# Kernel tuning notes

Measured on AMD Instinct MI355X. Metric: run time of the kernel, lower is better.

Reference implementation:

```python
import jax, jax.numpy as jnp
import numpy as np

B, Q, K = 8, 1024, 1024
DQ, DK, DV, H = 64, 64, 64, 64
NEG = -1000000.0


def setup_inputs() -> dict:
    key = jax.random.key(0)
    ks = jax.random.split(key, 7)
    return {
        "queries": jax.random.normal(ks[0], (B, Q, DQ), dtype=jnp.float32),
        "keys": jax.random.normal(ks[1], (B, K, DK), dtype=jnp.float32),
        "values": jax.random.normal(ks[2], (B, K, DV), dtype=jnp.float32),
        "valid_lens": jax.random.randint(ks[3], (B,), 1, K + 1, dtype=jnp.int64).astype(jnp.int32),
        # learned params (LazyLinear, no bias)
        "W_q": jax.random.normal(ks[4], (DQ, H), dtype=jnp.float32) / np.sqrt(DQ),
        "W_k": jax.random.normal(ks[5], (DK, H), dtype=jnp.float32) / np.sqrt(DK),
        "w_v": jax.random.normal(ks[6], (H,), dtype=jnp.float32) / np.sqrt(H),
    }


def reference(queries, keys, values, valid_lens, W_q, W_k, w_v):
    q = jnp.einsum("bqd,dh->bqh", queries, W_q)            # [B,Q,H]
    k = jnp.einsum("bkd,dh->bkh", keys, W_k)               # [B,K,H]
    # broadcast-add + tanh materializes [B,Q,K,H] (faithful to original)
    features = jnp.tanh(q[:, :, None, :] + k[:, None, :, :])
    scores = jnp.einsum("bqkh,h->bqk", features, w_v)      # [B,Q,K]
    # masked softmax: valid_lens is 1-D -> broadcast over query rows
    mask = jnp.arange(scores.shape[-1])[None, None, :] < valid_lens[:, None, None]
    scores = jnp.where(mask, scores, NEG)
    attn = jax.nn.softmax(scores, axis=-1)                 # [B,Q,K]
    return jnp.einsum("bqk,bkv->bqv", attn, values)        # [B,Q,DV]
```

## Files before the change

### kernel.cpp

```cpp
#include <hip/hip_runtime.h>

#define BDIM 8
#define QDIM 1024
#define KDIM 1024
#define HDIM 64
#define KTPC 2
#define MAXCH 8

constexpr float kLog2e = 1.4426950408889634f;
constexpr float kC2 = 2.0f * kLog2e;

__global__ __launch_bounds__(256) void proj_both(
    const float* __restrict__ queries, const float* __restrict__ keys,
    const float* __restrict__ Wq, const float* __restrict__ Wk,
    float* __restrict__ eq, float* __restrict__ ek) {
  const int bid = blockIdx.x;
  const bool isK = bid >= 128;
  const float* X = isK ? keys : queries;
  const float* W = isK ? Wk : Wq;
  float* Y = isK ? ek : eq;
  const long long base = (long long)(bid & 127) * 64 * 64;

  __shared__ __align__(16) float xs[64][68];
  __shared__ __align__(16) float ws[64][64];
  const int t = threadIdx.x;
  {
    const int r = t >> 4, sl = t & 15;
#pragma unroll
    for (int i = 0; i < 4; ++i) {
      *(float4*)&xs[r + i * 16][sl * 4] =
          *(const float4*)&X[base + (long long)(r + i * 16) * 64 + sl * 4];
      *(float4*)&ws[r + i * 16][sl * 4] =
          *(const float4*)&W[(r + i * 16) * 64 + sl * 4];
    }
  }
  __syncthreads();

  const int r = t >> 2;
  const int c0 = (t & 3) * 16;
  float acc[16];
#pragma unroll
  for (int j = 0; j < 16; ++j) acc[j] = 0.0f;

#pragma unroll 8
  for (int d = 0; d < 64; ++d) {
    const float xv = xs[r][d];
#pragma unroll
    for (int j4 = 0; j4 < 4; ++j4) {
      float4 w4 = *(float4*)&ws[d][c0 + j4 * 4];
      acc[j4 * 4 + 0] = fmaf(xv, w4.x, acc[j4 * 4 + 0]);
      acc[j4 * 4 + 1] = fmaf(xv, w4.y, acc[j4 * 4 + 1]);
      acc[j4 * 4 + 2] = fmaf(xv, w4.z, acc[j4 * 4 + 2]);
      acc[j4 * 4 + 3] = fmaf(xv, w4.w, acc[j4 * 4 + 3]);
    }
  }
#pragma unroll
  for (int j4 = 0; j4 < 4; ++j4) {
    float4 o = make_float4(
        fminf(__builtin_amdgcn_exp2f(acc[j4 * 4 + 0] * kC2), 32768.0f),
        fminf(__builtin_amdgcn_exp2f(acc[j4 * 4 + 1] * kC2), 32768.0f),
        fminf(__builtin_amdgcn_exp2f(acc[j4 * 4 + 2] * kC2), 32768.0f),
        fminf(__builtin_amdgcn_exp2f(acc[j4 * 4 + 3] * kC2), 32768.0f));
    *(float4*)&Y[base + (long long)r * 64 + c0 + j4 * 4] = o;
  }
}

__global__ __launch_bounds__(256, 3) void fused_kernel(
    const float* __restrict__ eqp, const float* __restrict__ ekp,
    const float* __restrict__ vglob, const float* __restrict__ wv,
    const int* __restrict__ vlens, float* __restrict__ part_o,
    float2* __restrict__ part_ml) {
  int pre[9];
  pre[0] = 0;
#pragma unroll
  for (int bb = 0; bb < 8; ++bb) {
    int nt = (vlens[bb] + 63) >> 6;
    nt = nt < 16 ? nt : 16;
    const int nch = (nt + KTPC - 1) / KTPC;
    pre[bb + 1] = pre[bb] + (nch << 6);
  }
  const int g = blockIdx.x;
  if (g >= pre[8]) return;
  int b = 0;
#pragma unroll
  for (int i = 0; i < 7; ++i) b += (g >= pre[i + 1]);
  const int local = g - pre[b];
  const int qt = local & 63;
  const int ch = local >> 6;
  const int q0 = qt * 16;
  const int vlen = vlens[b];
  int nt = (vlen + 63) >> 6;
  nt = nt < 16 ? nt : 16;
  const int kt0 = ch * KTPC;
  const int ktend = (kt0 + KTPC < nt) ? kt0 + KTPC : nt;

  __shared__ __align__(16) float qs[16][64];
  __shared__ __align__(16) float ks[64][64];
  __shared__ __align__(16) float vs[64][64];
  __shared__ __align__(16) float ps[16][68];
  const int t = threadIdx.x;
  const int tq = t >> 4;
  const int kg = t & 15;
  const int kbs = kg << 2;
  const int key0 = ((kbs + 0) ^ kg) & 15;
  const int key1 = ((kbs + 1) ^ kg) & 15;
  const int key2 = ((kbs + 2) ^ kg) & 15;
  const int key3 = ((kbs + 3) ^ kg) & 15;

  float sumw = 0.0f;
#pragma unroll
  for (int h = 0; h < 64; ++h) sumw += wv[h];

  {
    const int r = t >> 4, sl = t & 15;
    *(float4*)&qs[r][sl * 4] =
        *(const float4*)&eqp[(long long)(b * QDIM + q0 + r) * 64 + sl * 4];
  }

  float4 o4 = make_float4(0.0f, 0.0f, 0.0f, 0.0f);
  float m = -3.0e38f, l = 0.0f;

  for (int kt = kt0; kt < ktend; ++kt) {
    __syncthreads();
#pragma unroll
    for (int i = 0; i < 4; ++i) {
      const int f = i * 256 + t;
      const int k = f >> 4, sl = f & 15;
      const int key = (k ^ (k >> 2)) & 15;
      const long long grow = (long long)(b * KDIM + kt * 64 + k) * 64 + sl * 4;
      *(float4*)&ks[k][(sl ^ key) * 4] = *(const float4*)&ekp[grow];
      *(float4*)&vs[k][sl * 4] = *(const float4*)&vglob[grow];
    }
    __syncthreads();

    float acc0 = 0.0f, acc1 = 0.0f, acc2 = 0.0f, acc3 = 0.0f;
    float4 qA, kA0, kA1, kA2, kA3;
    float4 qB, kB0, kB1, kB2, kB3;

#define LOAD_STAGE(QF, K0, K1, K2, K3, H)                  \
  QF = *(const float4*)&qs[tq][(H) * 4];                   \
  K0 = *(const float4*)&ks[kbs + 0][((H) ^ key0) * 4];     \
  K1 = *(const float4*)&ks[kbs + 1][((H) ^ key1) * 4];     \
  K2 = *(const float4*)&ks[kbs + 2][((H) ^ key2) * 4];     \
  K3 = *(const float4*)&ks[kbs + 3][((H) ^ key3) * 4];

#define QUAD(ACC, QF, KF, W0, W1, W2, W3)                  \
  {                                                        \
    const float u0 = fmaf(QF.x, KF.x, 1.0f);               \
    const float u1 = fmaf(QF.y, KF.y, 1.0f);               \
    const float u2 = fmaf(QF.z, KF.z, 1.0f);               \
    const float u3 = fmaf(QF.w, KF.w, 1.0f);               \
    const float d01 = u0 * u1;                             \
    const float d23 = u2 * u3;                             \
    const float n01 = fmaf(W1, u0, W0 * u1);               \
    const float n23 = fmaf(W3, u2, W2 * u3);               \
    const float num = fmaf(n23, d01, n01 * d23);           \
    ACC = fmaf(num, __builtin_amdgcn_rcpf(d01 * d23), ACC);\
  }

#define COMP_STAGE(QF, K0, K1, K2, K3, H)                  \
  {                                                        \
    const float w0 = wv[(H) * 4 + 0];                      \
    const float w1 = wv[(H) * 4 + 1];                      \
    const float w2 = wv[(H) * 4 + 2];                      \
    const float w3 = wv[(H) * 4 + 3];                      \
    QUAD(acc0, QF, K0, w0, w1, w2, w3)                     \
    QUAD(acc1, QF, K1, w0, w1, w2, w3)                     \
    QUAD(acc2, QF, K2, w0, w1, w2, w3)                     \
    QUAD(acc3, QF, K3, w0, w1, w2, w3)                     \
  }

    LOAD_STAGE(qA, kA0, kA1, kA2, kA3, 0)
#pragma unroll
    for (int h = 0; h < 16; h += 2) {
      LOAD_STAGE(qB, kB0, kB1, kB2, kB3, h + 1)
      COMP_STAGE(qA, kA0, kA1, kA2, kA3, h)
      if (h + 2 < 16) LOAD_STAGE(qA, kA0, kA1, kA2, kA3, h + 2)
      COMP_STAGE(qB, kB0, kB1, kB2, kB3, h + 1)
    }
#undef LOAD_STAGE
#undef COMP_STAGE
#undef QUAD

    const int kgl = kt * 64 + kbs;
    float s0 = fmaf(-2.0f, acc0, sumw);
    float s1 = fmaf(-2.0f, acc1, sumw);
    float s2 = fmaf(-2.0f, acc2, sumw);
    float s3 = fmaf(-2.0f, acc3, sumw);
    s0 = (kgl + 0 < vlen) ? s0 : -3.0e38f;
    s1 = (kgl + 1 < vlen) ? s1 : -3.0e38f;
    s2 = (kgl + 2 < vlen) ? s2 : -3.0e38f;
    s3 = (kgl + 3 < vlen) ? s3 : -3.0e38f;
    float tm = fmaxf(fmaxf(s0, s1), fmaxf(s2, s3));
#pragma unroll
    for (int s = 1; s < 16; s <<= 1) tm = fmaxf(tm, __shfl_xor(tm, s, 64));
    const float mn = fmaxf(m, tm);
    const float scale = __builtin_amdgcn_exp2f((m - mn) * kLog2e);
    const float p0 = __builtin_amdgcn_exp2f((s0 - mn) * kLog2e);
    const float p1 = __builtin_amdgcn_exp2f((s1 - mn) * kLog2e);
    const float p2 = __builtin_amdgcn_exp2f((s2 - mn) * kLog2e);
    const float p3 = __builtin_amdgcn_exp2f((s3 - mn) * kLog2e);
    float tsum = (p0 + p1) + (p2 + p3);
#pragma unroll
    for (int s = 1; s < 16; s <<= 1) tsum += __shfl_xor(tsum, s, 64);
    l = fmaf(l, scale, tsum);
    m = mn;
    o4.x *= scale; o4.y *= scale; o4.z *= scale; o4.w *= scale;
    *(float4*)&ps[tq][kbs] = make_float4(p0, p1, p2, p3);
    __syncthreads();

#pragma unroll 4
    for (int k4 = 0; k4 < 16; ++k4) {
      const float4 p4 = *(const float4*)&ps[tq][k4 * 4];
      const float pw[4] = {p4.x, p4.y, p4.z, p4.w};
#pragma unroll
      for (int e = 0; e < 4; ++e) {
        const float4 vv = *(const float4*)&vs[k4 * 4 + e][kbs];
        o4.x = fmaf(pw[e], vv.x, o4.x);
        o4.y = fmaf(pw[e], vv.y, o4.y);
        o4.z = fmaf(pw[e], vv.z, o4.z);
        o4.w = fmaf(pw[e], vv.w, o4.w);
      }
    }
  }

  *(float4*)&part_o[((long long)g * 16 + tq) * 64 + kbs] = o4;
  if (kg == 0) part_ml[g * 16 + tq] = make_float2(m, l);
}

__global__ __launch_bounds__(256) void combine_kernel(
    const float* __restrict__ part_o, const float2* __restrict__ part_ml,
    const int* __restrict__ vlens, float* __restrict__ out) {
  int pre[8], nchv[8];
  int run = 0;
#pragma unroll
  for (int bb = 0; bb < 8; ++bb) {
    int nt = (vlens[bb] + 63) >> 6;
    nt = nt < 16 ? nt : 16;
    nchv[bb] = (nt + KTPC - 1) / KTPC;
    pre[bb] = run;
    run += nchv[bb] << 6;
  }
  const int t = threadIdx.x;
  const int row = blockIdx.x * 4 + (t >> 6);
  const int lane = t & 63;
  const int b = row >> 10;
  const int q = row & (QDIM - 1);
  const int qt = q >> 4;
  const int tq = q & 15;
  const int nch = nchv[b];
  const int slot0 = pre[b] + qt;

  float M = -3.0e38f;
  float mv[MAXCH], lv[MAXCH];
#pragma unroll
  for (int c = 0; c < MAXCH; ++c) {
    if (c < nch) {
      const float2 ml = part_ml[(slot0 + (c << 6)) * 16 + tq];
      mv[c] = ml.x;
      lv[c] = ml.y;
      M = fmaxf(M, ml.x);
    }
  }
  float L = 0.0f, acc = 0.0f;
#pragma unroll
  for (int c = 0; c < MAXCH; ++c) {
    if (c < nch) {
      const float w = __builtin_amdgcn_exp2f((mv[c] - M) * kLog2e);
      L = fmaf(lv[c], w, L);
      const float ov =
          part_o[((long long)(slot0 + (c << 6)) * 16 + tq) * 64 + lane];
      acc = fmaf(ov, w, acc);
    }
  }
  out[(long long)row * 64 + lane] = acc * __builtin_amdgcn_rcpf(L);
}

extern "C" void kernel_launch(void* const* d_in, const int* in_sizes, int n_in,
                              void* d_out, int out_size, void* d_ws, size_t ws_size,
                              hipStream_t stream) {
  const float* queries = (const float*)d_in[0];
  const float* keys    = (const float*)d_in[1];
  const float* values  = (const float*)d_in[2];
  const int*   vlens   = (const int*)d_in[3];
  const float* Wq      = (const float*)d_in[4];
  const float* Wk      = (const float*)d_in[5];
  const float* wv      = (const float*)d_in[6];
  float* out = (float*)d_out;

  float*  eq      = (float*)d_ws;
  float*  ek      = eq + (size_t)BDIM * QDIM * HDIM;
  float*  part_o  = ek + (size_t)BDIM * KDIM * HDIM;
  float2* part_ml = (float2*)(part_o + (size_t)4096 * 16 * 64);

  proj_both<<<dim3(256), 256, 0, stream>>>(queries, keys, Wq, Wk, eq, ek);
  fused_kernel<<<dim3(4096), 256, 0, stream>>>(eq, ek, values, wv, vlens,
                                               part_o, part_ml);
  combine_kernel<<<dim3(BDIM * QDIM / 4), 256, 0, stream>>>(part_o, part_ml,
                                                            vlens, out);
}
```

Baseline: 62.68 us.

## Replace online softmax max with static bound and drop rescaling and sync

Scores are a tanh sum weighted by w_v, so they are bounded above by sum|w_v|. The kernel now subtracts that bound as a fixed offset instead of tracking a running max. This removes the per-tile max shuffle, the rescale exponentials, a block barrier and the max bookkeeping in the combine kernel, which now just sums partial outputs and denominators. It also splits the projection kernel into twice as many smaller blocks, raises the occupancy hint on the fused kernel, and rotates the P-tile access pattern to spread LDS banks. The trade-off is a risk of exp underflow if the w_v magnitudes were large, and the P tile now relies on each row being written and read within a single wavefront without a barrier.

```diff
diff --git a/kernel.cpp b/kernel.cpp
--- a/kernel.cpp
+++ b/kernel.cpp
@@ -15,38 +15,39 @@
     const float* __restrict__ Wq, const float* __restrict__ Wk,
     float* __restrict__ eq, float* __restrict__ ek) {
   const int bid = blockIdx.x;
-  const bool isK = bid >= 128;
+  const bool isK = bid >= 256;
   const float* X = isK ? keys : queries;
   const float* W = isK ? Wk : Wq;
   float* Y = isK ? ek : eq;
-  const long long base = (long long)(bid & 127) * 64 * 64;
-
-  __shared__ __align__(16) float xs[64][68];
+  const long long base = (long long)(bid & 255) * 32 * 64;
+
+  __shared__ __align__(16) float xs[32][68];
   __shared__ __align__(16) float ws[64][64];
   const int t = threadIdx.x;
   {
     const int r = t >> 4, sl = t & 15;
 #pragma unroll
-    for (int i = 0; i < 4; ++i) {
+    for (int i = 0; i < 2; ++i)
       *(float4*)&xs[r + i * 16][sl * 4] =
           *(const float4*)&X[base + (long long)(r + i * 16) * 64 + sl * 4];
+#pragma unroll
+    for (int i = 0; i < 4; ++i)
       *(float4*)&ws[r + i * 16][sl * 4] =
           *(const float4*)&W[(r + i * 16) * 64 + sl * 4];
-    }
   }
   __syncthreads();
 
-  const int r = t >> 2;
-  const int c0 = (t & 3) * 16;
-  float acc[16];
-#pragma unroll
-  for (int j = 0; j < 16; ++j) acc[j] = 0.0f;
+  const int r = t >> 3;
+  const int c0 = (t & 7) * 8;
+  float acc[8];
+#pragma unroll
+  for (int j = 0; j < 8; ++j) acc[j] = 0.0f;
 
 #pragma unroll 8
   for (int d = 0; d < 64; ++d) {
     const float xv = xs[r][d];
 #pragma unroll
-    for (int j4 = 0; j4 < 4; ++j4) {
+    for (int j4 = 0; j4 < 2; ++j4) {
       float4 w4 = *(float4*)&ws[d][c0 + j4 * 4];
       acc[j4 * 4 + 0] = fmaf(xv, w4.x, acc[j4 * 4 + 0]);
       acc[j4 * 4 + 1] = fmaf(xv, w4.y, acc[j4 * 4 + 1]);
@@ -55,7 +56,7 @@
     }
   }
 #pragma unroll
-  for (int j4 = 0; j4 < 4; ++j4) {
+  for (int j4 = 0; j4 < 2; ++j4) {
     float4 o = make_float4(
         fminf(__builtin_amdgcn_exp2f(acc[j4 * 4 + 0] * kC2), 32768.0f),
         fminf(__builtin_amdgcn_exp2f(acc[j4 * 4 + 1] * kC2), 32768.0f),
@@ -65,11 +66,11 @@
   }
 }
 
-__global__ __launch_bounds__(256, 3) void fused_kernel(
+__global__ __launch_bounds__(256, 4) void fused_kernel(
     const float* __restrict__ eqp, const float* __restrict__ ekp,
     const float* __restrict__ vglob, const float* __restrict__ wv,
     const int* __restrict__ vlens, float* __restrict__ part_o,
-    float2* __restrict__ part_ml) {
+    float* __restrict__ part_l) {
   int pre[9];
   pre[0] = 0;
 #pragma unroll
@@ -97,7 +98,7 @@
   __shared__ __align__(16) float qs[16][64];
   __shared__ __align__(16) float ks[64][64];
   __shared__ __align__(16) float vs[64][64];
-  __shared__ __align__(16) float ps[16][68];
+  __shared__ __align__(16) float ps[16][64];
   const int t = threadIdx.x;
   const int tq = t >> 4;
   const int kg = t & 15;
@@ -107,9 +108,14 @@
   const int key2 = ((kbs + 2) ^ kg) & 15;
   const int key3 = ((kbs + 3) ^ kg) & 15;
 
-  float sumw = 0.0f;
-#pragma unroll
-  for (int h = 0; h < 64; ++h) sumw += wv[h];
+  float sumw = 0.0f, sumabs = 0.0f;
+#pragma unroll
+  for (int h = 0; h < 64; ++h) {
+    const float w = wv[h];
+    sumw += w;
+    sumabs += fabsf(w);
+  }
+  const float sbias = sumw - sumabs;
 
   {
     const int r = t >> 4, sl = t & 15;
@@ -118,7 +124,7 @@
   }
 
   float4 o4 = make_float4(0.0f, 0.0f, 0.0f, 0.0f);
-  float m = -3.0e38f, l = 0.0f;
+  float l = 0.0f;
 
   for (int kt = kt0; kt < ktend; ++kt) {
     __syncthreads();
@@ -183,39 +189,29 @@
 #undef QUAD
 
     const int kgl = kt * 64 + kbs;
-    float s0 = fmaf(-2.0f, acc0, sumw);
-    float s1 = fmaf(-2.0f, acc1, sumw);
-    float s2 = fmaf(-2.0f, acc2, sumw);
-    float s3 = fmaf(-2.0f, acc3, sumw);
+    float s0 = fmaf(-2.0f, acc0, sbias);
+    float s1 = fmaf(-2.0f, acc1, sbias);
+    float s2 = fmaf(-2.0f, acc2, sbias);
+    float s3 = fmaf(-2.0f, acc3, sbias);
     s0 = (kgl + 0 < vlen) ? s0 : -3.0e38f;
     s1 = (kgl + 1 < vlen) ? s1 : -3.0e38f;
     s2 = (kgl + 2 < vlen) ? s2 : -3.0e38f;
     s3 = (kgl + 3 < vlen) ? s3 : -3.0e38f;
-    float tm = fmaxf(fmaxf(s0, s1), fmaxf(s2, s3));
-#pragma unroll
-    for (int s = 1; s < 16; s <<= 1) tm = fmaxf(tm, __shfl_xor(tm, s, 64));
-    const float mn = fmaxf(m, tm);
-    const float scale = __builtin_amdgcn_exp2f((m - mn) * kLog2e);
-    const float p0 = __builtin_amdgcn_exp2f((s0 - mn) * kLog2e);
-    const float p1 = __builtin_amdgcn_exp2f((s1 - mn) * kLog2e);
-    const float p2 = __builtin_amdgcn_exp2f((s2 - mn) * kLog2e);
-    const float p3 = __builtin_amdgcn_exp2f((s3 - mn) * kLog2e);
-    float tsum = (p0 + p1) + (p2 + p3);
-#pragma unroll
-    for (int s = 1; s < 16; s <<= 1) tsum += __shfl_xor(tsum, s, 64);
-    l = fmaf(l, scale, tsum);
-    m = mn;
-    o4.x *= scale; o4.y *= scale; o4.z *= scale; o4.w *= scale;
-    *(float4*)&ps[tq][kbs] = make_float4(p0, p1, p2, p3);
-    __syncthreads();
+    const float p0 = __builtin_amdgcn_exp2f(s0 * kLog2e);
+    const float p1 = __builtin_amdgcn_exp2f(s1 * kLog2e);
+    const float p2 = __builtin_amdgcn_exp2f(s2 * kLog2e);
+    const float p3 = __builtin_amdgcn_exp2f(s3 * kLog2e);
+    l += (p0 + p1) + (p2 + p3);
+    *(float4*)&ps[tq][(((kg + tq) & 15)) * 4] = make_float4(p0, p1, p2, p3);
 
 #pragma unroll 4
     for (int k4 = 0; k4 < 16; ++k4) {
-      const float4 p4 = *(const float4*)&ps[tq][k4 * 4];
+      const int kk = (k4 + tq) & 15;
+      const float4 p4 = *(const float4*)&ps[tq][((kk + tq) & 15) * 4];
       const float pw[4] = {p4.x, p4.y, p4.z, p4.w};
 #pragma unroll
       for (int e = 0; e < 4; ++e) {
-        const float4 vv = *(const float4*)&vs[k4 * 4 + e][kbs];
+        const float4 vv = *(const float4*)&vs[kk * 4 + e][kbs];
         o4.x = fmaf(pw[e], vv.x, o4.x);
         o4.y = fmaf(pw[e], vv.y, o4.y);
         o4.z = fmaf(pw[e], vv.z, o4.z);
@@ -224,12 +220,14 @@
     }
   }
 
+#pragma unroll
+  for (int s = 1; s < 16; s <<= 1) l += __shfl_xor(l, s, 64);
   *(float4*)&part_o[((long long)g * 16 + tq) * 64 + kbs] = o4;
-  if (kg == 0) part_ml[g * 16 + tq] = make_float2(m, l);
+  if (kg == 0) part_l[g * 16 + tq] = l;
 }
 
 __global__ __launch_bounds__(256) void combine_kernel(
-    const float* __restrict__ part_o, const float2* __restrict__ part_ml,
+    const float* __restrict__ part_o, const float* __restrict__ part_l,
     const int* __restrict__ vlens, float* __restrict__ out) {
   int pre[8], nchv[8];
   int run = 0;
@@ -251,26 +249,12 @@
   const int nch = nchv[b];
   const int slot0 = pre[b] + qt;
 
-  float M = -3.0e38f;
-  float mv[MAXCH], lv[MAXCH];
+  float L = 0.0f, acc = 0.0f;
 #pragma unroll
   for (int c = 0; c < MAXCH; ++c) {
     if (c < nch) {
-      const float2 ml = part_ml[(slot0 + (c << 6)) * 16 + tq];
-      mv[c] = ml.x;
-      lv[c] = ml.y;
-      M = fmaxf(M, ml.x);
-    }
-  }
-  float L = 0.0f, acc = 0.0f;
-#pragma unroll
-  for (int c = 0; c < MAXCH; ++c) {
-    if (c < nch) {
-      const float w = __builtin_amdgcn_exp2f((mv[c] - M) * kLog2e);
-      L = fmaf(lv[c], w, L);
-      const float ov =
-          part_o[((long long)(slot0 + (c << 6)) * 16 + tq) * 64 + lane];
-      acc = fmaf(ov, w, acc);
+      L += part_l[(slot0 + (c << 6)) * 16 + tq];
+      acc += part_o[((long long)(slot0 + (c << 6)) * 16 + tq) * 64 + lane];
     }
   }
   out[(long long)row * 64 + lane] = acc * __builtin_amdgcn_rcpf(L);
@@ -288,14 +272,14 @@
   const float* wv      = (const float*)d_in[6];
   float* out = (float*)d_out;
 
-  float*  eq      = (float*)d_ws;
-  float*  ek      = eq + (size_t)BDIM * QDIM * HDIM;
-  float*  part_o  = ek + (size_t)BDIM * KDIM * HDIM;
-  float2* part_ml = (float2*)(part_o + (size_t)4096 * 16 * 64);
-
-  proj_both<<<dim3(256), 256, 0, stream>>>(queries, keys, Wq, Wk, eq, ek);
+  float* eq     = (float*)d_ws;
+  float* ek     = eq + (size_t)BDIM * QDIM * HDIM;
+  float* part_o = ek + (size_t)BDIM * KDIM * HDIM;
+  float* part_l = part_o + (size_t)4096 * 16 * 64;
+
+  proj_both<<<dim3(512), 256, 0, stream>>>(queries, keys, Wq, Wk, eq, ek);
   fused_kernel<<<dim3(4096), 256, 0, stream>>>(eq, ek, values, wv, vlens,
-                                               part_o, part_ml);
-  combine_kernel<<<dim3(BDIM * QDIM / 4), 256, 0, stream>>>(part_o, part_ml,
+                                               part_o, part_l);
+  combine_kernel<<<dim3(BDIM * QDIM / 4), 256, 0, stream>>>(part_o, part_l,
                                                             vlens, out);
 }
```

Result: faster. 54.85 us (-12.5%).
